# Kernel optimization log

Hardware: AMD Instinct MI355X
Metric: run time of the kernel (lower is better)

## Reference

```python
import jax, jax.numpy as jnp
import numpy as np

N = 50000
E = 800000
IN_C = 128
OUT_C = 128
EPS = 1e-5


def _w(key, i, o, scale=0.02):
    return jax.random.normal(key, (i, o), dtype=jnp.float32) * scale


def setup_inputs() -> dict:
    key = jax.random.key(0)
    ks = jax.random.split(key, 20)
    x = jax.random.normal(ks[0], (N, IN_C), dtype=jnp.float32)
    edge_index = jax.random.randint(ks[1], (2, E), 0, N, dtype=jnp.int64)
    C = OUT_C
    return {
        "x": x,
        "edge_index": edge_index,
        # conv1: SAGEConv(IN_C -> 2C): lin_l (neighbors, with bias), lin_r (root, no bias)
        "Wl1": _w(ks[2], IN_C, 2 * C), "bl1": jnp.zeros((2 * C,), jnp.float32),
        "Wr1": _w(ks[3], IN_C, 2 * C),
        "ln1_w": jnp.ones((2 * C,), jnp.float32), "ln1_b": jnp.zeros((2 * C,), jnp.float32),
        "W1": _w(ks[4], 2 * C, 4 * C), "b1": jnp.zeros((4 * C,), jnp.float32),
        "W2": _w(ks[5], 4 * C, 2 * C), "b2": jnp.zeros((2 * C,), jnp.float32),
        # conv2: SAGEConv(2C -> C)
        "Wl2": _w(ks[6], 2 * C, C), "bl2": jnp.zeros((C,), jnp.float32),
        "Wr2": _w(ks[7], 2 * C, C),
        "ln2_w": jnp.ones((C,), jnp.float32), "ln2_b": jnp.zeros((C,), jnp.float32),
        "W3": _w(ks[8], C, 2 * C), "b3": jnp.zeros((2 * C,), jnp.float32),
        "W4": _w(ks[9], 2 * C, C), "b4": jnp.zeros((C,), jnp.float32),
    }


def _sage_conv(x, src, dst, Wl, bl, Wr):
    # mean aggregation of source features at destination nodes
    n = x.shape[0]
    msg = x[src]                                              # [E, F]
    agg = jax.ops.segment_sum(msg, dst, num_segments=n)       # [N, F]
    deg = jax.ops.segment_sum(jnp.ones((src.shape[0], 1), x.dtype), dst, num_segments=n)
    agg = agg / jnp.maximum(deg, 1.0)                         # empty neighborhoods -> 0
    return agg @ Wl + bl + x @ Wr


def _graph_layernorm(x, w, b):
    # PyG LayerNorm mode='graph' (single graph): normalize over all nodes and features
    mu = x.mean()
    xc = x - mu
    var = (xc * xc).mean()
    return xc * jax.lax.rsqrt(var + EPS) * w + b


def reference(x, edge_index, Wl1, bl1, Wr1, ln1_w, ln1_b, W1, b1, W2, b2,
              Wl2, bl2, Wr2, ln2_w, ln2_b, W3, b3, W4, b4):
    src, dst = edge_index[0], edge_index[1]
    h = _sage_conv(x, src, dst, Wl1, bl1, Wr1)
    h = jax.nn.relu(_graph_layernorm(h, ln1_w, ln1_b))
    h = jax.nn.relu(h @ W1 + b1)
    h = jax.nn.relu(h @ W2 + b2)
    h = _sage_conv(h, src, dst, Wl2, bl2, Wr2)
    h = jax.nn.relu(_graph_layernorm(h, ln2_w, ln2_b))
    h = jax.nn.relu(h @ W3 + b3)
    return h @ W4 + b4
```

## Files before the change

### kernel.cpp

```cpp
#include <hip/hip_runtime.h>

#define NN   50000
#define EE   800000
#define MPAD 50048
#define NBUCK 196

typedef __bf16 bf16x8 __attribute__((ext_vector_type(8)));
typedef float  vfloat4 __attribute__((ext_vector_type(4)));
typedef short  vshort4 __attribute__((ext_vector_type(4)));
typedef short  vshort8 __attribute__((ext_vector_type(8)));

__device__ __forceinline__ short f2bf(float f) {
  union { float f; unsigned u; } v; v.f = f;
  unsigned r = v.u + 0x7FFFu + ((v.u >> 16) & 1u);
  return (short)(r >> 16);
}
__device__ __forceinline__ float bf2f(short h) {
  union { unsigned u; float f; } v; v.u = ((unsigned)(unsigned short)h) << 16;
  return v.f;
}

__device__ __forceinline__ void load_lds16(const short* g, short* l) {
  __builtin_amdgcn_global_load_lds(
      (__attribute__((address_space(1))) void*)(void*)g,
      (__attribute__((address_space(3))) void*)(void*)l, 16, 0, 0);
}

__global__ __launch_bounds__(256) void detect_kernel(const unsigned* __restrict__ e,
                                                     int* __restrict__ flag) {
  unsigned v = 0;
  for (int i = threadIdx.x; i < 2048; i += 256) v |= e[2 * i + 1];
  for (int o = 32; o; o >>= 1) v |= (unsigned)__shfl_down((int)v, o, 64);
  __shared__ unsigned r[4];
  if ((threadIdx.x & 63) == 0) r[threadIdx.x >> 6] = v;
  __syncthreads();
  if (threadIdx.x == 0) flag[0] = ((r[0] | r[1] | r[2] | r[3]) == 0) ? 1 : 0;
}


__global__ __launch_bounds__(256) void bin_count(const void* __restrict__ edges,
                                                 const int* __restrict__ flag,
                                                 int* __restrict__ bcnt) {
  __shared__ int h[NBUCK];
  int t = threadIdx.x;
  for (int i = t; i < NBUCK; i += 256) h[i] = 0;
  __syncthreads();
  const int per = (EE + NBUCK - 1) / NBUCK;
  int lo = blockIdx.x * per, hi = lo + per;
  if (hi > EE) hi = EE;
  int fl = flag[0];
  for (int e = lo + t; e < hi; e += 256) {
    int dv = fl ? (int)((const long long*)edges)[EE + e] : ((const int*)edges)[EE + e];
    atomicAdd(&h[dv >> 8], 1);
  }
  __syncthreads();
  for (int i = t; i < NBUCK; i += 256)
    if (h[i]) atomicAdd(&bcnt[i], h[i]);
}

__global__ __launch_bounds__(256) void bin_scan(const int* __restrict__ bcnt,
                                                int* __restrict__ bstart,
                                                int* __restrict__ bcur) {
  __shared__ int tmp[256];
  int t = threadIdx.x;
  int v = (t < NBUCK) ? bcnt[t] : 0;
  tmp[t] = v;
  __syncthreads();
  int acc = v;
  for (int d = 1; d < 256; d <<= 1) {
    int u = (t >= d) ? tmp[t - d] : 0;
    __syncthreads();
    acc += u;
    tmp[t] = acc;
    __syncthreads();
  }
  int excl = acc - v;
  if (t < NBUCK) { bstart[t] = excl; bcur[t] = excl; }
  if (t == NBUCK - 1) bstart[NBUCK] = excl + v;
}

__global__ __launch_bounds__(256) void bin_scatter(const void* __restrict__ edges,
                                                   const int* __restrict__ flag,
                                                   int* __restrict__ bcur,
                                                   long long* __restrict__ staging) {
  __shared__ int h[NBUCK];
  __shared__ int base[NBUCK];
  int t = threadIdx.x;
  for (int i = t; i < NBUCK; i += 256) h[i] = 0;
  __syncthreads();
  const int per = (EE + NBUCK - 1) / NBUCK;
  int lo = blockIdx.x * per, hi = lo + per;
  if (hi > EE) hi = EE;
  int fl = flag[0];
  for (int e = lo + t; e < hi; e += 256) {
    int dv = fl ? (int)((const long long*)edges)[EE + e] : ((const int*)edges)[EE + e];
    atomicAdd(&h[dv >> 8], 1);
  }
  __syncthreads();
  for (int i = t; i < NBUCK; i += 256) {
    int c = h[i];
    base[i] = c ? atomicAdd(&bcur[i], c) : 0;
    h[i] = 0;
  }
  __syncthreads();
  for (int e = lo + t; e < hi; e += 256) {
    int sv, dv;
    if (fl) { sv = (int)((const long long*)edges)[e]; dv = (int)((const long long*)edges)[EE + e]; }
    else    { sv = ((const int*)edges)[e];            dv = ((const int*)edges)[EE + e]; }
    int b = dv >> 8;
    int r = atomicAdd(&h[b], 1);
    staging[base[b] + r] = ((long long)sv << 32) | (unsigned)dv;
  }
}

__global__ __launch_bounds__(256) void bucket_csr(const int* __restrict__ bstart,
                                                  const long long* __restrict__ staging,
                                                  int* __restrict__ offs,
                                                  int* __restrict__ csr) {
  int b = blockIdx.x, t = threadIdx.x;
  int n0 = b << 8;
  int s0 = bstart[b], s1 = bstart[b + 1];
  __shared__ int cnt[256], tmp[256], cur[256];
  cnt[t] = 0;
  __syncthreads();
  for (int i = s0 + t; i < s1; i += 256)
    atomicAdd(&cnt[((int)(staging[i] & 0xffffffffLL)) - n0], 1);
  __syncthreads();
  int v = cnt[t];
  tmp[t] = v;
  __syncthreads();
  int acc = v;
  for (int d = 1; d < 256; d <<= 1) {
    int u = (t >= d) ? tmp[t - d] : 0;
    __syncthreads();
    acc += u;
    tmp[t] = acc;
    __syncthreads();
  }
  int excl = acc - v;
  int node = n0 + t;
  if (node < NN) offs[node] = s0 + excl;
  cur[t] = s0 + excl;
  __syncthreads();
  for (int i = s0 + t; i < s1; i += 256) {
    long long pk = staging[i];
    int dv = (int)(pk & 0xffffffffLL);
    int sv = (int)(pk >> 32);
    int p = atomicAdd(&cur[dv - n0], 1);
    csr[p] = sv;
  }
  if (b == 0 && t == 0) offs[NN] = EE;
}

__global__ __launch_bounds__(256) void xcast_kernel(const float* __restrict__ x,
                                                    short* __restrict__ xbf) {
  int i = blockIdx.x * 256 + threadIdx.x;
  if (i >= NN * 128 / 8) return;
  vfloat4 v0 = *(const vfloat4*)(x + (size_t)i * 8);
  vfloat4 v1 = *(const vfloat4*)(x + (size_t)i * 8 + 4);
  vshort8 o;
  o[0] = f2bf(v0.x); o[1] = f2bf(v0.y); o[2] = f2bf(v0.z); o[3] = f2bf(v0.w);
  o[4] = f2bf(v1.x); o[5] = f2bf(v1.y); o[6] = f2bf(v1.z); o[7] = f2bf(v1.w);
  *(vshort8*)(xbf + (size_t)i * 8) = o;
}

__global__ __launch_bounds__(256) void prep_all(
    const float* __restrict__ Wl1, const float* __restrict__ Wr1,
    const float* __restrict__ W1,  const float* __restrict__ W2,
    const float* __restrict__ Wl2, const float* __restrict__ Wr2,
    const float* __restrict__ W3,  const float* __restrict__ W4,
    short* __restrict__ wc1T, short* __restrict__ w1T, short* __restrict__ w2T,
    short* __restrict__ wlr2T, short* __restrict__ w3T, short* __restrict__ w4T) {
  int b = blockIdx.x;
  if (b >= 1280 && b < 1536) {
    int idx = (b - 1280) * 256 + threadIdx.x;
    int n = idx >> 8, k = idx & 255;
    float v = (n < 128) ? Wl2[(size_t)k * 128 + n] : Wr2[(size_t)k * 128 + (n - 128)];
    wlr2T[idx] = f2bf(v);
    return;
  }
  const float *s0, *s1; short* dst; int K0, logK, Nc, base;
  if      (b <  256) { s0=Wl1; s1=Wr1; dst=wc1T; K0=128; logK=8; Nc=256; base=0;    }
  else if (b <  768) { s0=W1;  s1=W1;  dst=w1T;  K0=256; logK=8; Nc=512; base=256;  }
  else if (b < 1280) { s0=W2;  s1=W2;  dst=w2T;  K0=512; logK=9; Nc=256; base=768;  }
  else if (b < 1664) { s0=W3;  s1=W3;  dst=w3T;  K0=128; logK=7; Nc=256; base=1536; }
  else               { s0=W4;  s1=W4;  dst=w4T;  K0=256; logK=8; Nc=128; base=1664; }
  int idx = (b - base) * 256 + threadIdx.x;
  int n = idx >> logK, k = idx & ((1 << logK) - 1);
  float v = (k < K0) ? s0[(size_t)k * Nc + n] : s1[(size_t)(k - K0) * Nc + n];
  dst[idx] = f2bf(v);
}

__global__ __launch_bounds__(256) void prep_bias(const float* __restrict__ bl2,
                                                 float* __restrict__ cbias) {
  int t = threadIdx.x;
  cbias[t] = (t < 128) ? 0.f : bl2[t - 128];
}

__global__ __launch_bounds__(256) void reduce_stats(const float* __restrict__ part,
                                                    int n, float* __restrict__ out) {
  float s = 0.f, s2 = 0.f;
  for (int i = threadIdx.x; i < n; i += 256) { s += part[2 * i]; s2 += part[2 * i + 1]; }
  for (int o = 32; o; o >>= 1) {
    s  += __shfl_down(s,  o, 64);
    s2 += __shfl_down(s2, o, 64);
  }
  __shared__ float ps[8];
  int lane = threadIdx.x & 63, wv = threadIdx.x >> 6;
  if (lane == 0) { ps[wv] = s; ps[wv + 4] = s2; }
  __syncthreads();
  if (threadIdx.x == 0) {
    out[0] = ps[0] + ps[1] + ps[2] + ps[3];
    out[1] = ps[4] + ps[5] + ps[6] + ps[7];
  }
}

template<int CONCAT>
__global__ __launch_bounds__(256) void agg_mean(const short* __restrict__ src,
                                                const int* __restrict__ offs,
                                                const int* __restrict__ csr,
                                                short* __restrict__ dst) {
  int node = blockIdx.x * 4 + (threadIdx.x >> 6);
  int lane = threadIdx.x & 63;
  if (node >= MPAD) return;
  short* row = dst + (size_t)node * (CONCAT ? 256 : 128);
  if (node >= NN) {
    if (CONCAT) *(vshort4*)(row + lane * 4) = (vshort4){0, 0, 0, 0};
    else if (lane < 32) *(vshort4*)(row + lane * 4) = (vshort4){0, 0, 0, 0};
    return;
  }
  int g = lane >> 4, sub = lane & 15;
  int e0 = offs[node], e1 = offs[node + 1];
  float a0[8] = {0, 0, 0, 0, 0, 0, 0, 0};
  float a1[8] = {0, 0, 0, 0, 0, 0, 0, 0};
  int e = e0;
  while (e < e1) {
    int cnt = e1 - e; if (cnt > 64) cnt = 64;
    int myidx = (lane < cnt) ? csr[e + lane] : 0;
    for (int i = 0; i < cnt; i += 8) {
      int p0 = g + i;
      int p1 = g + i + 4;
      int s0 = __shfl(myidx, p0, 64);
      int s1 = __shfl(myidx, p1, 64);
      if (p0 < cnt) {
        vshort8 v0 = *(const vshort8*)(src + (size_t)s0 * 128 + sub * 8);
#pragma unroll
        for (int j = 0; j < 8; j++) a0[j] += bf2f(v0[j]);
      }
      if (p1 < cnt) {
        vshort8 v1 = *(const vshort8*)(src + (size_t)s1 * 128 + sub * 8);
#pragma unroll
        for (int j = 0; j < 8; j++) a1[j] += bf2f(v1[j]);
      }
    }
    e += cnt;
  }
#pragma unroll
  for (int j = 0; j < 8; j++) {
    a0[j] += a1[j];
    a0[j] += __shfl_down(a0[j], 32, 64);
    a0[j] += __shfl_down(a0[j], 16, 64);
  }
  float inv = (e1 > e0) ? 1.f / (float)(e1 - e0) : 0.f;
  if (g == 0) {
    vshort8 o;
#pragma unroll
    for (int j = 0; j < 8; j++) o[j] = f2bf(a0[j] * inv);
    *(vshort8*)(row + sub * 8) = o;
  } else if (CONCAT && g == 1) {
    *(vshort8*)(row + 128 + sub * 8) = *(const vshort8*)(src + (size_t)node * 128 + sub * 8);
  }
}

__global__ __launch_bounds__(256) void add_stats(const short* __restrict__ r2,
                                                 const short* __restrict__ a2,
                                                 short* __restrict__ h_d,
                                                 float* __restrict__ partials) {
  int i = blockIdx.x * 256 + threadIdx.x;
  const int tot8 = MPAD * 128 / 8, real8 = NN * 128 / 8;
  float s = 0.f, s2 = 0.f;
  if (i < tot8) {
    if (i >= real8) {
      *(vshort8*)(h_d + (size_t)i * 8) = (vshort8){0,0,0,0,0,0,0,0};
    } else {
      vshort8 rv = *(const vshort8*)(r2 + (size_t)i * 8);
      vshort8 av = *(const vshort8*)(a2 + (size_t)i * 8);
      vshort8 o;
#pragma unroll
      for (int j = 0; j < 8; j++) {
        float v = bf2f(rv[j]) + bf2f(av[j]);
        s += v; s2 += v * v;
        o[j] = f2bf(v);
      }
      *(vshort8*)(h_d + (size_t)i * 8) = o;
    }
  }
  int lane = threadIdx.x & 63, wave = threadIdx.x >> 6;
  for (int o2 = 32; o2; o2 >>= 1) {
    s  += __shfl_down(s,  o2, 64);
    s2 += __shfl_down(s2, o2, 64);
  }
  __shared__ float ps[8];
  if (lane == 0) { ps[wave] = s; ps[wave + 4] = s2; }
  __syncthreads();
  if (threadIdx.x == 0) {
    partials[2 * blockIdx.x]     = ps[0] + ps[1] + ps[2] + ps[3];
    partials[2 * blockIdx.x + 1] = ps[4] + ps[5] + ps[6] + ps[7];
  }
}

__global__ __launch_bounds__(256) void ln_apply(const short* __restrict__ h,
                                                const float* __restrict__ stats,
                                                const float* __restrict__ w,
                                                const float* __restrict__ b,
                                                short* __restrict__ out,
                                                int realElems, int totElems, int F,
                                                float invCount) {
  int base = (blockIdx.x * blockDim.x + threadIdx.x) * 4;
  if (base >= totElems) return;
  if (base >= realElems) { *(vshort4*)(out + base) = (vshort4){0,0,0,0}; return; }
  float mu  = stats[0] * invCount;
  float var = stats[1] * invCount - mu * mu;
  float rs  = rsqrtf(var + 1e-5f);
  int col = base % F;
  vshort4 hv = *(const vshort4*)(h + base);
  vshort4 o;
  o.x = f2bf(fmaxf((bf2f(hv.x) - mu) * rs * w[col]     + b[col],     0.f));
  o.y = f2bf(fmaxf((bf2f(hv.y) - mu) * rs * w[col + 1] + b[col + 1], 0.f));
  o.z = f2bf(fmaxf((bf2f(hv.z) - mu) * rs * w[col + 2] + b[col + 2], 0.f));
  o.w = f2bf(fmaxf((bf2f(hv.w) - mu) * rs * w[col + 3] + b[col + 3], 0.f));
  *(vshort4*)(out + base) = o;
}

template<int RELU, int OUTBF, int BOUND, int STATS, int SPLIT>
__global__ __launch_bounds__(256) void gemm_bt(const short* __restrict__ A,
                                               const short* __restrict__ BT,
                                               const float* __restrict__ bias,
                                               float* __restrict__ Cf,
                                               short* __restrict__ Cb,
                                               short* __restrict__ Cb2,
                                               float* __restrict__ partials,
                                               int Nc, int K, int Mreal) {
  __shared__ short lsA[128 * 64];
  __shared__ short lsB[128 * 64];
  const int tid  = threadIdx.x;
  const int lane = tid & 63;
  const int wave = tid >> 6;
  const int wr   = (wave >> 1) << 6;
  const int wc   = (wave & 1) << 6;
  const int row0 = blockIdx.y << 7;
  const int col0 = blockIdx.x << 7;
  const int r16  = lane & 15;
  const int quad = lane >> 4;
  const int srow   = lane >> 3;
  const int schunk = lane & 7;
  const int sxoff  = ((schunk ^ srow) << 3);

  vfloat4 acc[4][4];
#pragma unroll
  for (int i = 0; i < 4; i++)
#pragma unroll
    for (int j = 0; j < 4; j++) acc[i][j] = (vfloat4){0.f, 0.f, 0.f, 0.f};

  for (int k0 = 0; k0 < K; k0 += 64) {
    __syncthreads();
#pragma unroll
    for (int t = 0; t < 4; t++) {
      int seg  = (wave << 2) + t;
      int trow = (seg << 3) + srow;
      load_lds16(A  + (size_t)(row0 + trow) * K + k0 + sxoff, lsA + (seg << 9) + lane * 8);
      load_lds16(BT + (size_t)(col0 + trow) * K + k0 + sxoff, lsB + (seg << 9) + lane * 8);
    }
    __syncthreads();
#pragma unroll
    for (int kk = 0; kk < 64; kk += 32) {
      int kf8 = (kk >> 3) + quad;
      bf16x8 af[4], bfr[4];
#pragma unroll
      for (int i = 0; i < 4; i++) {
        int r = wr + (i << 4) + r16;
        af[i] = *(const bf16x8*)(lsA + (r << 6) + ((kf8 ^ (r & 7)) << 3));
      }
#pragma unroll
      for (int j = 0; j < 4; j++) {
        int r = wc + (j << 4) + r16;
        bfr[j] = *(const bf16x8*)(lsB + (r << 6) + ((kf8 ^ (r & 7)) << 3));
      }
#pragma unroll
      for (int i = 0; i < 4; i++)
#pragma unroll
        for (int j = 0; j < 4; j++)
          acc[i][j] = __builtin_amdgcn_mfma_f32_16x16x32_bf16(bfr[j], af[i], acc[i][j], 0, 0, 0);
    }
  }

  float s = 0.f, s2 = 0.f;
#pragma unroll
  for (int i = 0; i < 4; i++) {
    int gr = row0 + wr + (i << 4) + r16;
    if (BOUND && gr >= Mreal) continue;
#pragma unroll
    for (int j = 0; j < 4; j++) {
      int gc = col0 + wc + (j << 4) + (quad << 2);
      vfloat4 bv = *(const vfloat4*)(bias + gc);
      vfloat4 v;
#pragma unroll
      for (int p = 0; p < 4; p++) {
        float t = acc[i][j][p] + bv[p];
        if (STATS) { s += t; s2 += t * t; }
        if (RELU) t = fmaxf(t, 0.f);
        v[p] = t;
      }
      if (OUTBF) {
        vshort4 o;
#pragma unroll
        for (int p = 0; p < 4; p++) o[p] = f2bf(v[p]);
        if (SPLIT) {
          if (gc < 128) *(vshort4*)(Cb  + (size_t)gr * 128 + gc)       = o;
          else          *(vshort4*)(Cb2 + (size_t)gr * 128 + gc - 128) = o;
        } else {
          *(vshort4*)(Cb + (size_t)gr * Nc + gc) = o;
        }
      } else {
        *(vfloat4*)(Cf + (size_t)gr * Nc + gc) = v;
      }
    }
  }
  if (STATS) {
    for (int o2 = 32; o2; o2 >>= 1) {
      s  += __shfl_down(s,  o2, 64);
      s2 += __shfl_down(s2, o2, 64);
    }
    __shared__ float ps[8];
    if (lane == 0) { ps[wave] = s; ps[wave + 4] = s2; }
    __syncthreads();
    if (tid == 0) {
      int bid = blockIdx.y * gridDim.x + blockIdx.x;
      partials[2 * bid]     = ps[0] + ps[1] + ps[2] + ps[3];
      partials[2 * bid + 1] = ps[4] + ps[5] + ps[6] + ps[7];
    }
  }
}

extern "C" void kernel_launch(void* const* d_in, const int* in_sizes, int n_in,
                              void* d_out, int out_size, void* d_ws, size_t ws_size,
                              hipStream_t stream) {
  const float* x    = (const float*)d_in[0];
  const void*  edge = d_in[1];
  const float* Wl1  = (const float*)d_in[2];
  const float* bl1  = (const float*)d_in[3];
  const float* Wr1  = (const float*)d_in[4];
  const float* ln1w = (const float*)d_in[5];
  const float* ln1b = (const float*)d_in[6];
  const float* W1   = (const float*)d_in[7];
  const float* b1   = (const float*)d_in[8];
  const float* W2   = (const float*)d_in[9];
  const float* b2   = (const float*)d_in[10];
  const float* Wl2  = (const float*)d_in[11];
  const float* bl2  = (const float*)d_in[12];
  const float* Wr2  = (const float*)d_in[13];
  const float* ln2w = (const float*)d_in[14];
  const float* ln2b = (const float*)d_in[15];
  const float* W3   = (const float*)d_in[16];
  const float* b3   = (const float*)d_in[17];
  const float* W4   = (const float*)d_in[18];
  const float* b4   = (const float*)d_in[19];
  float* out = (float*)d_out;

  char* wsp = (char*)d_ws;
  size_t o = 0;
  auto alloc = [&](size_t bytes) -> void* {
    void* p = wsp + o;
    o = (o + bytes + 255) & ~(size_t)255;
    return p;
  };
  int*   flag   = (int*)alloc(4);
  int*   bcnt   = (int*)alloc(NBUCK * 4);
  int*   bstart = (int*)alloc((NBUCK + 1) * 4);
  int*   bcur   = (int*)alloc(NBUCK * 4);
  int*   offs   = (int*)alloc((size_t)(NN + 1) * 4);
  int*   csr    = (int*)alloc((size_t)EE * 4);
  long long* staging = (long long*)alloc((size_t)EE * 8);
  float* stats  = (float*)alloc(32);
  float* cbias  = (float*)alloc(256 * 4);
  float* pb1    = (float*)alloc(782 * 2 * 4);
  float* pb2    = (float*)alloc(3128 * 2 * 4);
  short* wc1T   = (short*)alloc(256 * 256 * 2);
  short* w1T    = (short*)alloc(512 * 256 * 2);
  short* w2T    = (short*)alloc(256 * 512 * 2);
  short* wlr2T  = (short*)alloc(256 * 256 * 2);
  short* w3T    = (short*)alloc(256 * 128 * 2);
  short* w4T    = (short*)alloc(128 * 256 * 2);
  char*  bufB   = (char*)alloc((size_t)MPAD * 512);
  char*  bufA   = (char*)alloc((size_t)MPAD * 1024);

  const size_t Q = (size_t)MPAD * 256;
  short* xbf = (short*)bufA;
  short* h1  = (short*)bufA;
  short* h_b = (short*)bufA;
  short* p2  = (short*)bufA;
  short* r2  = (short*)(bufA + Q);
  short* a2  = (short*)(bufA + 2 * Q);
  short* h_d = (short*)(bufA + 3 * Q);
  short* h_e = (short*)bufA;
  short* h_f = (short*)(bufA + Q);
  short* hcat1 = (short*)bufB;
  short* h_a   = (short*)bufB;
  short* h_c   = (short*)bufB;

  hipMemsetAsync(bcnt, 0, NBUCK * 4, stream);
  detect_kernel<<<1, 256, 0, stream>>>((const unsigned*)edge, flag);
  bin_count<<<NBUCK, 256, 0, stream>>>(edge, flag, bcnt);
  bin_scan<<<1, 256, 0, stream>>>(bcnt, bstart, bcur);
  bin_scatter<<<NBUCK, 256, 0, stream>>>(edge, flag, bcur, staging);
  bucket_csr<<<NBUCK, 256, 0, stream>>>(bstart, staging, offs, csr);

  xcast_kernel<<<(NN * 128 / 8 + 255) / 256, 256, 0, stream>>>(x, xbf);
  prep_all<<<1792, 256, 0, stream>>>(Wl1, Wr1, W1, W2, Wl2, Wr2, W3, W4,
                                     wc1T, w1T, w2T, wlr2T, w3T, w4T);
  prep_bias<<<1, 256, 0, stream>>>(bl2, cbias);

  agg_mean<1><<<MPAD / 4, 256, 0, stream>>>(xbf, offs, csr, hcat1);
  gemm_bt<0, 1, 1, 1, 0><<<dim3(2, MPAD / 128), 256, 0, stream>>>(
      hcat1, wc1T, bl1, nullptr, h1, nullptr, pb1, 256, 256, NN);
  reduce_stats<<<1, 256, 0, stream>>>(pb1, 782, stats);
  ln_apply<<<(MPAD * 256 / 4 + 255) / 256, 256, 0, stream>>>(
      h1, stats, ln1w, ln1b, h_a, NN * 256, MPAD * 256, 256, 1.f / (NN * 256.f));
  gemm_bt<1, 1, 0, 0, 0><<<dim3(4, MPAD / 128), 256, 0, stream>>>(
      h_a, w1T, b1, nullptr, h_b, nullptr, nullptr, 512, 256, MPAD);
  gemm_bt<1, 1, 0, 0, 0><<<dim3(2, MPAD / 128), 256, 0, stream>>>(
      h_b, w2T, b2, nullptr, h_c, nullptr, nullptr, 256, 512, MPAD);

  gemm_bt<0, 1, 0, 0, 1><<<dim3(2, MPAD / 128), 256, 0, stream>>>(
      h_c, wlr2T, cbias, nullptr, p2, r2, nullptr, 256, 256, MPAD);
  agg_mean<0><<<MPAD / 4, 256, 0, stream>>>(p2, offs, csr, a2);
  add_stats<<<MPAD * 128 / 8 / 256, 256, 0, stream>>>(r2, a2, h_d, pb2);
  reduce_stats<<<1, 256, 0, stream>>>(pb2, 3128, stats + 2);
  ln_apply<<<(MPAD * 128 / 4 + 255) / 256, 256, 0, stream>>>(
      h_d, stats + 2, ln2w, ln2b, h_e, NN * 128, MPAD * 128, 128, 1.f / (NN * 128.f));
  gemm_bt<1, 1, 0, 0, 0><<<dim3(2, MPAD / 128), 256, 0, stream>>>(
      h_e, w3T, b3, nullptr, h_f, nullptr, nullptr, 256, 128, MPAD);
  gemm_bt<0, 0, 1, 0, 0><<<dim3(1, MPAD / 128), 256, 0, stream>>>(
      h_f, w4T, b4, out, nullptr, nullptr, nullptr, 128, 256, NN);
}
```

Before: 403.0 us.

## Fuse back-to-back MLP GEMM pairs keeping intermediate activations in LDS

Adds a fused_mlp kernel that computes relu(A@W1+b1) one 128-column chunk at a time into shared memory, then immediately multiplies that chunk by the second weight matrix, accumulating the final output in registers. It replaces the two pairs of separate GEMM launches (W1/W2 and W3/W4). The goal is to avoid writing and re-reading the wide intermediate activations (512 and 256 columns) in global memory and to cut launches. In exchange, each block computes all output columns with large register accumulators, grid parallelism drops to about 391 blocks, and loads are not double-buffered. Workspace buffers are reassigned to match.

```diff
diff --git a/kernel.cpp b/kernel.cpp
--- a/kernel.cpp
+++ b/kernel.cpp
@@ -36,7 +36,6 @@
   __syncthreads();
   if (threadIdx.x == 0) flag[0] = ((r[0] | r[1] | r[2] | r[3]) == 0) ? 1 : 0;
 }
-
 
 __global__ __launch_bounds__(256) void bin_count(const void* __restrict__ edges,
                                                  const int* __restrict__ flag,
@@ -438,6 +437,150 @@
       int bid = blockIdx.y * gridDim.x + blockIdx.x;
       partials[2 * bid]     = ps[0] + ps[1] + ps[2] + ps[3];
       partials[2 * bid + 1] = ps[4] + ps[5] + ps[6] + ps[7];
+    }
+  }
+}
+
+template<int K1, int N1, int N2, int RELU2, int OUTBF, int BOUND>
+__global__ __launch_bounds__(256, 2) void fused_mlp(
+    const short* __restrict__ A,
+    const short* __restrict__ B1T, const float* __restrict__ bias1,
+    const short* __restrict__ B2T, const float* __restrict__ bias2,
+    short* __restrict__ Cb, float* __restrict__ Cf, int Mreal) {
+  constexpr int J2 = N2 / 32;
+  __shared__ short hmid[128 * 128];
+  __shared__ short stg[16384];
+  short* lsA  = stg;
+  short* lsB1 = stg + 8192;
+  short* lsB2 = stg;
+  const int tid  = threadIdx.x;
+  const int lane = tid & 63;
+  const int wave = tid >> 6;
+  const int wr   = (wave >> 1) << 6;
+  const int wc1  = (wave & 1) << 6;
+  const int wc2  = (wave & 1) * (N2 / 2);
+  const int row0 = blockIdx.x << 7;
+  const int r16  = lane & 15;
+  const int quad = lane >> 4;
+  const int srow   = lane >> 3;
+  const int schunk = lane & 7;
+  const int sxoff  = ((schunk ^ srow) << 3);
+
+  vfloat4 acc2[4][J2];
+#pragma unroll
+  for (int i = 0; i < 4; i++)
+#pragma unroll
+    for (int j = 0; j < J2; j++) acc2[i][j] = (vfloat4){0.f, 0.f, 0.f, 0.f};
+
+#pragma unroll 1
+  for (int cc = 0; cc < N1 / 128; cc++) {
+    vfloat4 acc1[4][4];
+#pragma unroll
+    for (int i = 0; i < 4; i++)
+#pragma unroll
+      for (int j = 0; j < 4; j++) acc1[i][j] = (vfloat4){0.f, 0.f, 0.f, 0.f};
+#pragma unroll 1
+    for (int k0 = 0; k0 < K1; k0 += 64) {
+      __syncthreads();
+#pragma unroll
+      for (int t = 0; t < 4; t++) {
+        int seg  = (wave << 2) + t;
+        int trow = (seg << 3) + srow;
+        load_lds16(A   + (size_t)(row0 + trow) * K1 + k0 + sxoff,     lsA  + (seg << 9) + lane * 8);
+        load_lds16(B1T + (size_t)(cc * 128 + trow) * K1 + k0 + sxoff, lsB1 + (seg << 9) + lane * 8);
+      }
+      __syncthreads();
+#pragma unroll
+      for (int kk = 0; kk < 64; kk += 32) {
+        int kf8 = (kk >> 3) + quad;
+        bf16x8 af[4], bfr[4];
+#pragma unroll
+        for (int i = 0; i < 4; i++) {
+          int r = wr + (i << 4) + r16;
+          af[i] = *(const bf16x8*)(lsA + (r << 6) + ((kf8 ^ (r & 7)) << 3));
+        }
+#pragma unroll
+        for (int j = 0; j < 4; j++) {
+          int r = wc1 + (j << 4) + r16;
+          bfr[j] = *(const bf16x8*)(lsB1 + (r << 6) + ((kf8 ^ (r & 7)) << 3));
+        }
+#pragma unroll
+        for (int i = 0; i < 4; i++)
+#pragma unroll
+          for (int j = 0; j < 4; j++)
+            acc1[i][j] = __builtin_amdgcn_mfma_f32_16x16x32_bf16(bfr[j], af[i], acc1[i][j], 0, 0, 0);
+      }
+    }
+#pragma unroll
+    for (int i = 0; i < 4; i++) {
+      int rr = wr + (i << 4) + r16;
+#pragma unroll
+      for (int j = 0; j < 4; j++) {
+        int ccol = wc1 + (j << 4) + (quad << 2);
+        vfloat4 bv = *(const vfloat4*)(bias1 + cc * 128 + ccol);
+        vshort4 o;
+#pragma unroll
+        for (int p = 0; p < 4; p++) o[p] = f2bf(fmaxf(acc1[i][j][p] + bv[p], 0.f));
+        int c8 = ccol >> 3;
+        *(vshort4*)(hmid + rr * 128 + ((c8 ^ (rr & 7)) << 3) + (quad & 1) * 4) = o;
+      }
+    }
+#pragma unroll 1
+    for (int kk2 = 0; kk2 < 128; kk2 += 64) {
+      __syncthreads();
+#pragma unroll
+      for (int t = 0; t < N2 / 32; t++) {
+        int seg  = wave * (N2 / 32) + t;
+        int trow = (seg << 3) + srow;
+        load_lds16(B2T + (size_t)trow * N1 + cc * 128 + kk2 + sxoff, lsB2 + (seg << 9) + lane * 8);
+      }
+      __syncthreads();
+#pragma unroll
+      for (int kk = 0; kk < 64; kk += 32) {
+        int kf8l = (kk >> 3) + quad;
+        int hc8  = ((kk2 + kk) >> 3) + quad;
+        bf16x8 af2[4], bfr2[J2];
+#pragma unroll
+        for (int i = 0; i < 4; i++) {
+          int rr = wr + (i << 4) + r16;
+          af2[i] = *(const bf16x8*)(hmid + rr * 128 + ((hc8 ^ (rr & 7)) << 3));
+        }
+#pragma unroll
+        for (int j = 0; j < J2; j++) {
+          int r = wc2 + (j << 4) + r16;
+          bfr2[j] = *(const bf16x8*)(lsB2 + (r << 6) + ((kf8l ^ (r & 7)) << 3));
+        }
+#pragma unroll
+        for (int i = 0; i < 4; i++)
+#pragma unroll
+          for (int j = 0; j < J2; j++)
+            acc2[i][j] = __builtin_amdgcn_mfma_f32_16x16x32_bf16(bfr2[j], af2[i], acc2[i][j], 0, 0, 0);
+      }
+    }
+  }
+#pragma unroll
+  for (int i = 0; i < 4; i++) {
+    int gr = row0 + wr + (i << 4) + r16;
+    if (BOUND && gr >= Mreal) continue;
+#pragma unroll
+    for (int j = 0; j < J2; j++) {
+      int gc = wc2 + (j << 4) + (quad << 2);
+      vfloat4 bv = *(const vfloat4*)(bias2 + gc);
+      vfloat4 v;
+#pragma unroll
+      for (int p = 0; p < 4; p++) {
+        float t = acc2[i][j][p] + bv[p];
+        if (RELU2) t = fmaxf(t, 0.f);
+        v[p] = t;
+      }
+      if (OUTBF) {
+        vshort4 o;
+#pragma unroll
+        for (int p = 0; p < 4; p++) o[p] = f2bf(v[p]);
+        *(vshort4*)(Cb + (size_t)gr * N2 + gc) = o;
+      } else {
+        *(vfloat4*)(Cf + (size_t)gr * N2 + gc) = v;
+      }
     }
   }
 }
@@ -497,16 +640,14 @@
   const size_t Q = (size_t)MPAD * 256;
   short* xbf = (short*)bufA;
   short* h1  = (short*)bufA;
-  short* h_b = (short*)bufA;
-  short* p2  = (short*)bufA;
-  short* r2  = (short*)(bufA + Q);
-  short* a2  = (short*)(bufA + 2 * Q);
-  short* h_d = (short*)(bufA + 3 * Q);
-  short* h_e = (short*)bufA;
-  short* h_f = (short*)(bufA + Q);
+  short* h_c = (short*)bufA;
+  short* p2  = (short*)(bufA + 2 * Q);
+  short* r2  = (short*)(bufA + 3 * Q);
+  short* h_d = (short*)bufA;
+  short* h_e = (short*)(bufA + Q);
   short* hcat1 = (short*)bufB;
   short* h_a   = (short*)bufB;
-  short* h_c   = (short*)bufB;
+  short* a2    = (short*)bufB;
 
   hipMemsetAsync(bcnt, 0, NBUCK * 4, stream);
   detect_kernel<<<1, 256, 0, stream>>>((const unsigned*)edge, flag);
@@ -526,10 +667,8 @@
   reduce_stats<<<1, 256, 0, stream>>>(pb1, 782, stats);
   ln_apply<<<(MPAD * 256 / 4 + 255) / 256, 256, 0, stream>>>(
       h1, stats, ln1w, ln1b, h_a, NN * 256, MPAD * 256, 256, 1.f / (NN * 256.f));
-  gemm_bt<1, 1, 0, 0, 0><<<dim3(4, MPAD / 128), 256, 0, stream>>>(
-      h_a, w1T, b1, nullptr, h_b, nullptr, nullptr, 512, 256, MPAD);
-  gemm_bt<1, 1, 0, 0, 0><<<dim3(2, MPAD / 128), 256, 0, stream>>>(
-      h_b, w2T, b2, nullptr, h_c, nullptr, nullptr, 256, 512, MPAD);
+  fused_mlp<256, 512, 256, 1, 1, 0><<<MPAD / 128, 256, 0, stream>>>(
+      h_a, w1T, b1, w2T, b2, h_c, nullptr, MPAD);
 
   gemm_bt<0, 1, 0, 0, 1><<<dim3(2, MPAD / 128), 256, 0, stream>>>(
       h_c, wlr2T, cbias, nullptr, p2, r2, nullptr, 256, 256, MPAD);
@@ -538,8 +677,6 @@
   reduce_stats<<<1, 256, 0, stream>>>(pb2, 3128, stats + 2);
   ln_apply<<<(MPAD * 128 / 4 + 255) / 256, 256, 0, stream>>>(
       h_d, stats + 2, ln2w, ln2b, h_e, NN * 128, MPAD * 128, 128, 1.f / (NN * 128.f));
-  gemm_bt<1, 1, 0, 0, 0><<<dim3(2, MPAD / 128), 256, 0, stream>>>(
-      h_e, w3T, b3, nullptr, h_f, nullptr, nullptr, 256, 128, MPAD);
-  gemm_bt<0, 0, 1, 0, 0><<<dim3(1, MPAD / 128), 256, 0, stream>>>(
-      h_f, w4T, b4, out, nullptr, nullptr, nullptr, 128, 256, NN);
-}
+  fused_mlp<128, 256, 128, 0, 0, 1><<<MPAD / 128, 256, 0, stream>>>(
+      h_e, w3T, b3, w4T, b4, nullptr, out, NN);
+}
```

After: 381.4 us. -5.4%, faster.
